# Kernel tuning notes

Hardware: AMD Instinct MI355X
Metric: run time of the kernel (lower is better)

## Reference

```python
import jax, jax.numpy as jnp
import numpy as np

D_MODEL = 64
NUM_MODES = 16
SCALE = 1.0 / (D_MODEL * D_MODEL)


def setup_inputs() -> dict:
    key = jax.random.key(0)
    kq, kk, kv = jax.random.split(key, 3)
    shape = (4, 2048, 64, 64)  # (b, t, c, mw_dim)
    q = jax.random.normal(kq, shape, dtype=jnp.float32)
    k = jax.random.normal(kk, shape, dtype=jnp.float32)
    v = jax.random.normal(kv, shape, dtype=jnp.float32)
    return {"q": q, "k": k, "v": v}


def reference(q, k, v):
    b, t, c, mw = q.shape
    modes = min(t // 2, NUM_MODES)
    # permute (b,t,c,mw) -> (b,h,d,t) with h=mw_dim, d=c
    xq = jnp.transpose(q, (0, 3, 2, 1))
    xk = jnp.transpose(k, (0, 3, 2, 1))
    xv = jnp.transpose(v, (0, 3, 2, 1))
    # rfft over time, keep lowest `modes` frequency bins (contiguous low-pass)
    qf = jnp.fft.rfft(xq, axis=-1)[..., :modes]  # (b,h,d,modes) complex64
    kf = jnp.fft.rfft(xk, axis=-1)[..., :modes]
    vf = jnp.fft.rfft(xv, axis=-1)[..., :modes]
    # complex-domain attention over the reduced mode set
    qk = jnp.einsum('bhdx,bhdy->bhxy', qf, kf)  # (b,h,modes,modes)
    qk = jnp.tanh(qk)  # complex tanh, matching torch.tanh on cfloat
    qkv = jnp.einsum('bhxy,bhdy->bhdx', qk, vf)  # (b,h,d,modes)
    # scatter back into full rfft spectrum (zeros elsewhere)
    out_ft = jnp.zeros((b, mw, c, t // 2 + 1), dtype=qkv.dtype)
    out_ft = out_ft.at[..., :modes].set(qkv)
    out = jnp.fft.irfft(out_ft * SCALE, n=t, axis=-1)  # (b,h,d,t) float32
    return jnp.transpose(out, (0, 3, 2, 1))  # (b,t,c,mw)
```

## Files before the change

kernel.cpp:

```cpp
#include <hip/hip_runtime.h>
#include <hip/hip_bf16.h>
#include <math.h>


#define T_DIM 2048
#define DH 4096
#define DH2 2048
#define CH 8
#define TPCH 64
#define TT 32

__global__ void init_tables(float* __restrict__ WA, float* __restrict__ Bt2) {
    int i = blockIdx.x * 256 + threadIdx.x;
    const float TWO_PI = 6.2831853071795864769f;
    if (i < 512 * 32) {
        int t = i >> 5, r = i & 31, m = r >> 1;
        int ph = (m * t) & 2047;
        float ang = TWO_PI * (float)ph * (1.0f / 2048.0f);
        WA[i] = (r & 1) ? sinf(ang) : cosf(ang);
    }
    int i2 = i - 512 * 32;
    if (i2 >= 0 && i2 < 1024 * 32) {
        int t = i2 >> 5, r = i2 & 31, m = r >> 1;
        int ph = (m * t) & 2047;
        float ang = TWO_PI * (float)ph * (1.0f / 2048.0f);
        const float S2 = 1.0f / (4096.0f * 2048.0f);
        float coef = (m == 0 ? 1.0f : 2.0f) * S2;
        float val;
        if (!(r & 1)) val = coef * cosf(ang);
        else          val = (m == 0) ? 0.0f : -coef * sinf(ang);
        Bt2[i2] = val;
    }
}

__global__ __launch_bounds__(256) void stageA(
        const float* __restrict__ q, const float* __restrict__ k,
        const float* __restrict__ v, const float* __restrict__ WA,
        float* __restrict__ P) {
    __shared__ float w[TPCH * 32];
    int tid = threadIdx.x;
    int c   = blockIdx.y;
    int tz  = blockIdx.z;
    int tensor = tz >> 2, b = tz & 3;

    #pragma unroll
    for (int it = 0; it < TPCH * 32 / 256; it++)
        w[it * 256 + tid] = WA[c * (TPCH * 32) + it * 256 + tid];
    __syncthreads();

    int dh2 = blockIdx.x * 256 + tid;
    const float* srcf = (tensor == 0 ? q : tensor == 1 ? k : v)
                        + (size_t)b * T_DIM * DH;
    const float2* p0 = (const float2*)srcf + (size_t)(c * TPCH) * DH2 + dh2;

    float2 accR[16], accI[16];
    #pragma unroll
    for (int m = 0; m < 16; m++) {
        accR[m] = make_float2(0.f, 0.f);
        accI[m] = make_float2(0.f, 0.f);
    }

    #pragma unroll 2
    for (int tl = 0; tl < TPCH; tl++) {
        float2 x0 = p0[(size_t)tl * DH2];
        float2 x1 = p0[(size_t)(tl + 512) * DH2];
        float2 x2 = p0[(size_t)(tl + 1024) * DH2];
        float2 x3 = p0[(size_t)(tl + 1536) * DH2];
        float2 u0 = make_float2(x0.x + x2.x, x0.y + x2.y);
        float2 u1 = make_float2(x1.x + x3.x, x1.y + x3.y);
        float2 d0 = make_float2(x0.x - x2.x, x0.y - x2.y);
        float2 d1 = make_float2(x1.x - x3.x, x1.y - x3.y);
        float2 e  = make_float2(u0.x + u1.x, u0.y + u1.y);
        float2 f  = make_float2(u0.x - u1.x, u0.y - u1.y);
        const float* ww = &w[tl * 32];
        #pragma unroll
        for (int m = 0; m < 16; m++) {
            float cm = ww[2 * m], sm = ww[2 * m + 1];
            if ((m & 3) == 0) {
                accR[m].x = fmaf(cm, e.x, accR[m].x);
                accR[m].y = fmaf(cm, e.y, accR[m].y);
                accI[m].x = fmaf(-sm, e.x, accI[m].x);
                accI[m].y = fmaf(-sm, e.y, accI[m].y);
            } else if ((m & 3) == 2) {
                accR[m].x = fmaf(cm, f.x, accR[m].x);
                accR[m].y = fmaf(cm, f.y, accR[m].y);
                accI[m].x = fmaf(-sm, f.x, accI[m].x);
                accI[m].y = fmaf(-sm, f.y, accI[m].y);
            } else if ((m & 3) == 1) {
                accR[m].x = fmaf(cm, d0.x, fmaf(-sm, d1.x, accR[m].x));
                accR[m].y = fmaf(cm, d0.y, fmaf(-sm, d1.y, accR[m].y));
                accI[m].x = fmaf(-sm, d0.x, fmaf(-cm, d1.x, accI[m].x));
                accI[m].y = fmaf(-sm, d0.y, fmaf(-cm, d1.y, accI[m].y));
            } else {
                accR[m].x = fmaf(cm, d0.x, fmaf(sm, d1.x, accR[m].x));
                accR[m].y = fmaf(cm, d0.y, fmaf(sm, d1.y, accR[m].y));
                accI[m].x = fmaf(-sm, d0.x, fmaf(cm, d1.x, accI[m].x));
                accI[m].y = fmaf(-sm, d0.y, fmaf(cm, d1.y, accI[m].y));
            }
        }
    }
    float2* pp = (float2*)P + (((size_t)tz * CH + c) * 32) * DH2 + dh2;
    #pragma unroll
    for (int m = 0; m < 16; m++) {
        pp[(size_t)m * DH2]        = accR[m];
        pp[(size_t)(16 + m) * DH2] = accI[m];
    }
}

__global__ __launch_bounds__(256) void reduceP(const float4* __restrict__ P,
                                               float4* __restrict__ Y) {
    size_t i   = (size_t)blockIdx.x * 256 + threadIdx.x;
    size_t tzj = i >> 10;
    size_t dh4 = i & 1023;
    size_t tz  = tzj >> 5;
    size_t j   = tzj & 31;
    const float4* p = P + ((tz * CH) * 32 + j) * 1024 + dh4;
    float4 s = make_float4(0.f, 0.f, 0.f, 0.f);
    #pragma unroll
    for (int cc = 0; cc < CH; cc++) {
        float4 t = p[(size_t)cc * 32 * 1024];
        s.x += t.x; s.y += t.y; s.z += t.z; s.w += t.w;
    }
    Y[i] = s;
}

__global__ __launch_bounds__(256) void stageB(const float* __restrict__ Y,
                                              float* __restrict__ G) {
    __shared__ float qf[64 * 33];
    __shared__ float kf[64 * 33];
    __shared__ float vf[64 * 33];
    __shared__ float qkr[16 * 17];
    __shared__ float qki[16 * 17];

    int tid = threadIdx.x;
    int bh  = blockIdx.x;
    int b   = bh >> 6;
    int h   = bh & 63;

    #pragma unroll
    for (int tensor = 0; tensor < 3; tensor++) {
        float* dst = (tensor == 0 ? qf : tensor == 1 ? kf : vf);
        const float* yp = Y + ((size_t)(tensor * 4 + b) * 32) * DH + h;
        #pragma unroll
        for (int it = 0; it < 8; it++) {
            int p = it * 256 + tid;
            int d = p & 63, j = p >> 6;
            dst[d * 33 + j] = yp[(size_t)j * DH + d * 64];
        }
    }
    __syncthreads();

    int x = tid >> 4, y = tid & 15;
    float ar = 0.f, ai = 0.f;
    #pragma unroll 4
    for (int d = 0; d < 64; d++) {
        float qr = qf[d * 33 + x],      qi = qf[d * 33 + 16 + x];
        float kr = kf[d * 33 + y],      ki = kf[d * 33 + 16 + y];
        ar += qr * kr - qi * ki;
        ai += qr * ki + qi * kr;
    }
    float re, im;
    float a2 = 2.f * ar, b2 = 2.f * ai;
    if (fabsf(a2) < 80.f) {
        float den = coshf(a2) + cosf(b2);
        re = sinhf(a2) / den;
        im = sinf(b2) / den;
    } else {
        re = copysignf(1.f, ar);
        im = 0.f;
    }
    qkr[x * 17 + y] = re;
    qki[x * 17 + y] = im;
    __syncthreads();

    int xx = tid & 15, db = tid >> 4;
    #pragma unroll
    for (int i = 0; i < 4; i++) {
        int d = db + i * 16;
        float cr = 0.f, ci = 0.f;
        #pragma unroll
        for (int yy = 0; yy < 16; yy++) {
            float tr = qkr[xx * 17 + yy], ti = qki[xx * 17 + yy];
            float vr = vf[d * 33 + yy],   vi = vf[d * 33 + 16 + yy];
            cr += tr * vr - ti * vi;
            ci += tr * vi + ti * vr;
        }
        G[((size_t)b * 32 + xx) * DH + d * 64 + h]      = cr;
        G[((size_t)b * 32 + 16 + xx) * DH + d * 64 + h] = ci;
    }
}

__global__ __launch_bounds__(256) void stageC(const float* __restrict__ G,
                                              const float* __restrict__ Bt2,
                                              float* __restrict__ out) {
    __shared__ float w[TT * 32];
    int tid = threadIdx.x;
    int c   = blockIdx.y;
    int b   = blockIdx.z;

    #pragma unroll
    for (int it = 0; it < TT * 32 / 256; it++)
        w[it * 256 + tid] = Bt2[c * (TT * 32) + it * 256 + tid];
    __syncthreads();

    int dh2 = blockIdx.x * 256 + tid;
    float2 gr[16], gi[16];
    const float2* gp = (const float2*)G + (size_t)b * 32 * DH2 + dh2;
    #pragma unroll
    for (int m = 0; m < 16; m++) {
        gr[m] = gp[(size_t)m * DH2];
        gi[m] = gp[(size_t)(16 + m) * DH2];
    }

    float2* o0 = (float2*)out + ((size_t)b * T_DIM + (size_t)c * TT) * DH2 + dh2;
    #pragma unroll 2
    for (int tl = 0; tl < TT; tl++) {
        const float* ww = &w[tl * 32];
        float2 E = make_float2(0.f, 0.f), O = make_float2(0.f, 0.f);
        #pragma unroll
        for (int m = 0; m < 16; m += 2) {
            E.x = fmaf(ww[2 * m],     gr[m].x, E.x);
            E.x = fmaf(ww[2 * m + 1], gi[m].x, E.x);
            E.y = fmaf(ww[2 * m],     gr[m].y, E.y);
            E.y = fmaf(ww[2 * m + 1], gi[m].y, E.y);
        }
        #pragma unroll
        for (int m = 1; m < 16; m += 2) {
            O.x = fmaf(ww[2 * m],     gr[m].x, O.x);
            O.x = fmaf(ww[2 * m + 1], gi[m].x, O.x);
            O.y = fmaf(ww[2 * m],     gr[m].y, O.y);
            O.y = fmaf(ww[2 * m + 1], gi[m].y, O.y);
        }
        o0[(size_t)tl * DH2] = make_float2(E.x + O.x, E.y + O.y);
        o0[(size_t)(tl + 1024) * DH2] = make_float2(E.x - O.x, E.y - O.y);
    }
}

extern "C" void kernel_launch(void* const* d_in, const int* in_sizes, int n_in,
                              void* d_out, int out_size, void* d_ws, size_t ws_size,
                              hipStream_t stream) {
    const float* q = (const float*)d_in[0];
    const float* k = (const float*)d_in[1];
    const float* v = (const float*)d_in[2];
    float* out = (float*)d_out;

    char* ws = (char*)d_ws;
    float* WA  = (float*)ws;
    float* Bt2 = (float*)(ws + 65536);
    float* P   = (float*)(ws + 65536 + 131072);
    float* Y   = (float*)(ws + 65536 + 131072 + 50331648);
    float* G   = (float*)(ws + 65536 + 131072 + 50331648 + 6291456);

    init_tables<<<192, 256, 0, stream>>>(WA, Bt2);
    stageA<<<dim3(8, CH, 12), 256, 0, stream>>>(q, k, v, WA, P);
    reduceP<<<1536, 256, 0, stream>>>((const float4*)P, (float4*)Y);
    stageB<<<256, 256, 0, stream>>>(Y, G);
    stageC<<<dim3(8, 32, 4), 256, 0, stream>>>(G, Bt2, out);
}
```

Before: 448.6 us.

## Increase stageA/stageC grid parallelism and prefetch stageA inputs

StageA is templated on the number of time chunks and launches 16 chunks when the workspace allows it, falling back to 8 otherwise. Its loop now loads the next timestep's inputs before computing the current one, and occupancy hints are added. StageC's time tile is halved so it launches twice as many blocks. The larger split doubles the partial-sum buffer, so reduceP has more memory to read and write.

```diff
diff --git a/kernel.cpp b/kernel.cpp
--- a/kernel.cpp
+++ b/kernel.cpp
@@ -6,9 +6,7 @@
 #define T_DIM 2048
 #define DH 4096
 #define DH2 2048
-#define CH 8
-#define TPCH 64
-#define TT 32
+#define TT 16
 
 __global__ void init_tables(float* __restrict__ WA, float* __restrict__ Bt2) {
     int i = blockIdx.x * 256 + threadIdx.x;
@@ -33,25 +31,62 @@
     }
 }
 
-__global__ __launch_bounds__(256) void stageA(
+#define STAGEA_BODY(TL) do {                                                   \
+    float2 u0 = make_float2(x0.x + x2.x, x0.y + x2.y);                         \
+    float2 u1 = make_float2(x1.x + x3.x, x1.y + x3.y);                         \
+    float2 d0 = make_float2(x0.x - x2.x, x0.y - x2.y);                         \
+    float2 d1 = make_float2(x1.x - x3.x, x1.y - x3.y);                         \
+    float2 e  = make_float2(u0.x + u1.x, u0.y + u1.y);                         \
+    float2 f  = make_float2(u0.x - u1.x, u0.y - u1.y);                         \
+    const float* ww = &w[(TL) * 32];                                           \
+    _Pragma("unroll")                                                          \
+    for (int m = 0; m < 16; m++) {                                             \
+        float cm = ww[2 * m], sm = ww[2 * m + 1];                              \
+        if ((m & 3) == 0) {                                                    \
+            accR[m].x = fmaf(cm, e.x, accR[m].x);                              \
+            accR[m].y = fmaf(cm, e.y, accR[m].y);                              \
+            accI[m].x = fmaf(-sm, e.x, accI[m].x);                             \
+            accI[m].y = fmaf(-sm, e.y, accI[m].y);                             \
+        } else if ((m & 3) == 2) {                                             \
+            accR[m].x = fmaf(cm, f.x, accR[m].x);                              \
+            accR[m].y = fmaf(cm, f.y, accR[m].y);                              \
+            accI[m].x = fmaf(-sm, f.x, accI[m].x);                             \
+            accI[m].y = fmaf(-sm, f.y, accI[m].y);                             \
+        } else if ((m & 3) == 1) {                                             \
+            accR[m].x = fmaf(cm, d0.x, fmaf(-sm, d1.x, accR[m].x));            \
+            accR[m].y = fmaf(cm, d0.y, fmaf(-sm, d1.y, accR[m].y));            \
+            accI[m].x = fmaf(-sm, d0.x, fmaf(-cm, d1.x, accI[m].x));           \
+            accI[m].y = fmaf(-sm, d0.y, fmaf(-cm, d1.y, accI[m].y));           \
+        } else {                                                               \
+            accR[m].x = fmaf(cm, d0.x, fmaf(sm, d1.x, accR[m].x));             \
+            accR[m].y = fmaf(cm, d0.y, fmaf(sm, d1.y, accR[m].y));             \
+            accI[m].x = fmaf(-sm, d0.x, fmaf(cm, d1.x, accI[m].x));            \
+            accI[m].y = fmaf(-sm, d0.y, fmaf(cm, d1.y, accI[m].y));            \
+        }                                                                      \
+    }                                                                          \
+} while (0)
+
+template <int CH_>
+__global__ __launch_bounds__(256, 5) void stageA(
         const float* __restrict__ q, const float* __restrict__ k,
         const float* __restrict__ v, const float* __restrict__ WA,
         float* __restrict__ P) {
-    __shared__ float w[TPCH * 32];
+    constexpr int TPCH_ = 512 / CH_;
+    __shared__ float w[TPCH_ * 32];
     int tid = threadIdx.x;
     int c   = blockIdx.y;
     int tz  = blockIdx.z;
     int tensor = tz >> 2, b = tz & 3;
 
     #pragma unroll
-    for (int it = 0; it < TPCH * 32 / 256; it++)
-        w[it * 256 + tid] = WA[c * (TPCH * 32) + it * 256 + tid];
+    for (int it = 0; it < TPCH_ * 32 / 256; it++)
+        w[it * 256 + tid] = WA[c * (TPCH_ * 32) + it * 256 + tid];
     __syncthreads();
 
     int dh2 = blockIdx.x * 256 + tid;
     const float* srcf = (tensor == 0 ? q : tensor == 1 ? k : v)
                         + (size_t)b * T_DIM * DH;
-    const float2* p0 = (const float2*)srcf + (size_t)(c * TPCH) * DH2 + dh2;
+    const float2* p0 = (const float2*)srcf + (size_t)(c * TPCH_) * DH2 + dh2;
 
     float2 accR[16], accI[16];
     #pragma unroll
@@ -60,46 +95,24 @@
         accI[m] = make_float2(0.f, 0.f);
     }
 
+    float2 x0 = p0[0];
+    float2 x1 = p0[(size_t)512 * DH2];
+    float2 x2 = p0[(size_t)1024 * DH2];
+    float2 x3 = p0[(size_t)1536 * DH2];
+
     #pragma unroll 2
-    for (int tl = 0; tl < TPCH; tl++) {
-        float2 x0 = p0[(size_t)tl * DH2];
-        float2 x1 = p0[(size_t)(tl + 512) * DH2];
-        float2 x2 = p0[(size_t)(tl + 1024) * DH2];
-        float2 x3 = p0[(size_t)(tl + 1536) * DH2];
-        float2 u0 = make_float2(x0.x + x2.x, x0.y + x2.y);
-        float2 u1 = make_float2(x1.x + x3.x, x1.y + x3.y);
-        float2 d0 = make_float2(x0.x - x2.x, x0.y - x2.y);
-        float2 d1 = make_float2(x1.x - x3.x, x1.y - x3.y);
-        float2 e  = make_float2(u0.x + u1.x, u0.y + u1.y);
-        float2 f  = make_float2(u0.x - u1.x, u0.y - u1.y);
-        const float* ww = &w[tl * 32];
-        #pragma unroll
-        for (int m = 0; m < 16; m++) {
-            float cm = ww[2 * m], sm = ww[2 * m + 1];
-            if ((m & 3) == 0) {
-                accR[m].x = fmaf(cm, e.x, accR[m].x);
-                accR[m].y = fmaf(cm, e.y, accR[m].y);
-                accI[m].x = fmaf(-sm, e.x, accI[m].x);
-                accI[m].y = fmaf(-sm, e.y, accI[m].y);
-            } else if ((m & 3) == 2) {
-                accR[m].x = fmaf(cm, f.x, accR[m].x);
-                accR[m].y = fmaf(cm, f.y, accR[m].y);
-                accI[m].x = fmaf(-sm, f.x, accI[m].x);
-                accI[m].y = fmaf(-sm, f.y, accI[m].y);
-            } else if ((m & 3) == 1) {
-                accR[m].x = fmaf(cm, d0.x, fmaf(-sm, d1.x, accR[m].x));
-                accR[m].y = fmaf(cm, d0.y, fmaf(-sm, d1.y, accR[m].y));
-                accI[m].x = fmaf(-sm, d0.x, fmaf(-cm, d1.x, accI[m].x));
-                accI[m].y = fmaf(-sm, d0.y, fmaf(-cm, d1.y, accI[m].y));
-            } else {
-                accR[m].x = fmaf(cm, d0.x, fmaf(sm, d1.x, accR[m].x));
-                accR[m].y = fmaf(cm, d0.y, fmaf(sm, d1.y, accR[m].y));
-                accI[m].x = fmaf(-sm, d0.x, fmaf(cm, d1.x, accI[m].x));
-                accI[m].y = fmaf(-sm, d0.y, fmaf(cm, d1.y, accI[m].y));
-            }
-        }
-    }
-    float2* pp = (float2*)P + (((size_t)tz * CH + c) * 32) * DH2 + dh2;
+    for (int tl = 0; tl < TPCH_ - 1; tl++) {
+        const float2* pn = p0 + (size_t)(tl + 1) * DH2;
+        float2 n0 = pn[0];
+        float2 n1 = pn[(size_t)512 * DH2];
+        float2 n2 = pn[(size_t)1024 * DH2];
+        float2 n3 = pn[(size_t)1536 * DH2];
+        STAGEA_BODY(tl);
+        x0 = n0; x1 = n1; x2 = n2; x3 = n3;
+    }
+    STAGEA_BODY(TPCH_ - 1);
+
+    float2* pp = (float2*)P + (((size_t)tz * CH_ + c) * 32) * DH2 + dh2;
     #pragma unroll
     for (int m = 0; m < 16; m++) {
         pp[(size_t)m * DH2]        = accR[m];
@@ -107,6 +120,7 @@
     }
 }
 
+template <int CH_>
 __global__ __launch_bounds__(256) void reduceP(const float4* __restrict__ P,
                                                float4* __restrict__ Y) {
     size_t i   = (size_t)blockIdx.x * 256 + threadIdx.x;
@@ -114,10 +128,10 @@
     size_t dh4 = i & 1023;
     size_t tz  = tzj >> 5;
     size_t j   = tzj & 31;
-    const float4* p = P + ((tz * CH) * 32 + j) * 1024 + dh4;
+    const float4* p = P + ((tz * CH_) * 32 + j) * 1024 + dh4;
     float4 s = make_float4(0.f, 0.f, 0.f, 0.f);
     #pragma unroll
-    for (int cc = 0; cc < CH; cc++) {
+    for (int cc = 0; cc < CH_; cc++) {
         float4 t = p[(size_t)cc * 32 * 1024];
         s.x += t.x; s.y += t.y; s.z += t.z; s.w += t.w;
     }
@@ -190,9 +204,9 @@
     }
 }
 
-__global__ __launch_bounds__(256) void stageC(const float* __restrict__ G,
-                                              const float* __restrict__ Bt2,
-                                              float* __restrict__ out) {
+__global__ __launch_bounds__(256, 6) void stageC(const float* __restrict__ G,
+                                                 const float* __restrict__ Bt2,
+                                                 float* __restrict__ out) {
     __shared__ float w[TT * 32];
     int tid = threadIdx.x;
     int c   = blockIdx.y;
@@ -247,13 +261,26 @@
     char* ws = (char*)d_ws;
     float* WA  = (float*)ws;
     float* Bt2 = (float*)(ws + 65536);
-    float* P   = (float*)(ws + 65536 + 131072);
-    float* Y   = (float*)(ws + 65536 + 131072 + 50331648);
-    float* G   = (float*)(ws + 65536 + 131072 + 50331648 + 6291456);
+    const size_t base = 65536 + 131072;
+
+    const size_t psz16 = (size_t)12 * 16 * 32 * DH * 4;
+    const size_t psz8  = (size_t)12 *  8 * 32 * DH * 4;
+    const size_t ysz   = 6291456, gsz = 2097152;
+    const bool big = ws_size >= base + psz16 + ysz + gsz;
+
+    size_t psz = big ? psz16 : psz8;
+    float* P = (float*)(ws + base);
+    float* Y = (float*)(ws + base + psz);
+    float* G = (float*)(ws + base + psz + ysz);
 
     init_tables<<<192, 256, 0, stream>>>(WA, Bt2);
-    stageA<<<dim3(8, CH, 12), 256, 0, stream>>>(q, k, v, WA, P);
-    reduceP<<<1536, 256, 0, stream>>>((const float4*)P, (float4*)Y);
+    if (big) {
+        stageA<16><<<dim3(8, 16, 12), 256, 0, stream>>>(q, k, v, WA, P);
+        reduceP<16><<<1536, 256, 0, stream>>>((const float4*)P, (float4*)Y);
+    } else {
+        stageA<8><<<dim3(8, 8, 12), 256, 0, stream>>>(q, k, v, WA, P);
+        reduceP<8><<<1536, 256, 0, stream>>>((const float4*)P, (float4*)Y);
+    }
     stageB<<<256, 256, 0, stream>>>(Y, G);
-    stageC<<<dim3(8, 32, 4), 256, 0, stream>>>(G, Bt2, out);
-}
+    stageC<<<dim3(8, 64, 4), 256, 0, stream>>>(G, Bt2, out);
+}
```

New measurement: 1.290 ms. 188% more time.

## Restructure stageA with float4 loads, LDS double-buffered butterflies, and more blocks

Applied to the files above, without the earlier changes.

StageA now has each wave load float4 rows for a different time step, do the radix-4 butterfly once, and stage the e/f/d0/d1 results in a double-buffered LDS array. Each thread then accumulates one scalar column across the four time steps while the next phase's global loads are in flight. Twiddles are read straight from global memory instead of being staged in shared memory. The grid doubles to 16 blocks per channel with half the accumulators per thread, and stageC's TT is halved with twice the y-blocks. This trades more syncthreads and LDS traffic for wider loads, lower register pressure and more parallelism.

```diff
diff --git a/kernel.cpp b/kernel.cpp
--- a/kernel.cpp
+++ b/kernel.cpp
@@ -8,7 +8,16 @@
 #define DH2 2048
 #define CH 8
 #define TPCH 64
-#define TT 32
+#define NT 4
+#define NPH (TPCH / NT)
+#define TT 16
+
+__device__ inline float4 f4add(float4 a, float4 b) {
+    return make_float4(a.x + b.x, a.y + b.y, a.z + b.z, a.w + b.w);
+}
+__device__ inline float4 f4sub(float4 a, float4 b) {
+    return make_float4(a.x - b.x, a.y - b.y, a.z - b.z, a.w - b.w);
+}
 
 __global__ void init_tables(float* __restrict__ WA, float* __restrict__ Bt2) {
     int i = blockIdx.x * 256 + threadIdx.x;
@@ -37,73 +46,93 @@
         const float* __restrict__ q, const float* __restrict__ k,
         const float* __restrict__ v, const float* __restrict__ WA,
         float* __restrict__ P) {
-    __shared__ float w[TPCH * 32];
-    int tid = threadIdx.x;
-    int c   = blockIdx.y;
-    int tz  = blockIdx.z;
+    __shared__ float elds[2][NT][4][256];
+
+    int tid  = threadIdx.x;
+    int bx   = blockIdx.x;
+    int c    = blockIdx.y;
+    int tz   = blockIdx.z;
     int tensor = tz >> 2, b = tz & 3;
-
-    #pragma unroll
-    for (int it = 0; it < TPCH * 32 / 256; it++)
-        w[it * 256 + tid] = WA[c * (TPCH * 32) + it * 256 + tid];
-    __syncthreads();
-
-    int dh2 = blockIdx.x * 256 + tid;
+    int iw   = tid >> 6;
+    int lane = tid & 63;
+
     const float* srcf = (tensor == 0 ? q : tensor == 1 ? k : v)
                         + (size_t)b * T_DIM * DH;
-    const float2* p0 = (const float2*)srcf + (size_t)(c * TPCH) * DH2 + dh2;
-
-    float2 accR[16], accI[16];
+    const float4* src4 = (const float4*)srcf;
+    int f4base = bx * 64 + lane;
+
+    float accR[16], accI[16];
+    #pragma unroll
+    for (int m = 0; m < 16; m++) { accR[m] = 0.f; accI[m] = 0.f; }
+
+    {
+        int t0 = c * TPCH + iw;
+        float4 x0 = src4[(size_t)t0 * 1024 + f4base];
+        float4 x1 = src4[(size_t)(t0 + 512) * 1024 + f4base];
+        float4 x2 = src4[(size_t)(t0 + 1024) * 1024 + f4base];
+        float4 x3 = src4[(size_t)(t0 + 1536) * 1024 + f4base];
+        float4 u0 = f4add(x0, x2), u1 = f4add(x1, x3);
+        float4 dd0 = f4sub(x0, x2), dd1 = f4sub(x1, x3);
+        ((float4*)&elds[0][iw][0][0])[lane] = f4add(u0, u1);
+        ((float4*)&elds[0][iw][1][0])[lane] = f4sub(u0, u1);
+        ((float4*)&elds[0][iw][2][0])[lane] = dd0;
+        ((float4*)&elds[0][iw][3][0])[lane] = dd1;
+    }
+    __syncthreads();
+
+    for (int ph = 0; ph < NPH; ph++) {
+        float4 n0, n1, n2, n3;
+        const bool has_next = (ph < NPH - 1);
+        if (has_next) {
+            int t0 = c * TPCH + (ph + 1) * NT + iw;
+            n0 = src4[(size_t)t0 * 1024 + f4base];
+            n1 = src4[(size_t)(t0 + 512) * 1024 + f4base];
+            n2 = src4[(size_t)(t0 + 1024) * 1024 + f4base];
+            n3 = src4[(size_t)(t0 + 1536) * 1024 + f4base];
+        }
+        int bsel = ph & 1;
+        #pragma unroll
+        for (int i = 0; i < NT; i++) {
+            float ee  = elds[bsel][i][0][tid];
+            float ff  = elds[bsel][i][1][tid];
+            float dd0 = elds[bsel][i][2][tid];
+            float dd1 = elds[bsel][i][3][tid];
+            const float* tw = WA + (size_t)(c * TPCH + ph * NT + i) * 32;
+            #pragma unroll
+            for (int m = 0; m < 16; m++) {
+                float cm = tw[2 * m], sm = tw[2 * m + 1];
+                if ((m & 3) == 0) {
+                    accR[m] = fmaf(cm, ee, accR[m]);
+                    accI[m] = fmaf(-sm, ee, accI[m]);
+                } else if ((m & 3) == 2) {
+                    accR[m] = fmaf(cm, ff, accR[m]);
+                    accI[m] = fmaf(-sm, ff, accI[m]);
+                } else if ((m & 3) == 1) {
+                    accR[m] = fmaf(cm, dd0, fmaf(-sm, dd1, accR[m]));
+                    accI[m] = fmaf(-sm, dd0, fmaf(-cm, dd1, accI[m]));
+                } else {
+                    accR[m] = fmaf(cm, dd0, fmaf(sm, dd1, accR[m]));
+                    accI[m] = fmaf(-sm, dd0, fmaf(cm, dd1, accI[m]));
+                }
+            }
+        }
+        if (has_next) {
+            int nb = (ph + 1) & 1;
+            float4 u0 = f4add(n0, n2), u1 = f4add(n1, n3);
+            float4 dd0 = f4sub(n0, n2), dd1 = f4sub(n1, n3);
+            ((float4*)&elds[nb][iw][0][0])[lane] = f4add(u0, u1);
+            ((float4*)&elds[nb][iw][1][0])[lane] = f4sub(u0, u1);
+            ((float4*)&elds[nb][iw][2][0])[lane] = dd0;
+            ((float4*)&elds[nb][iw][3][0])[lane] = dd1;
+            __syncthreads();
+        }
+    }
+
+    float* pp = P + ((size_t)(tz * CH + c) * 32) * DH + bx * 256 + tid;
     #pragma unroll
     for (int m = 0; m < 16; m++) {
-        accR[m] = make_float2(0.f, 0.f);
-        accI[m] = make_float2(0.f, 0.f);
-    }
-
-    #pragma unroll 2
-    for (int tl = 0; tl < TPCH; tl++) {
-        float2 x0 = p0[(size_t)tl * DH2];
-        float2 x1 = p0[(size_t)(tl + 512) * DH2];
-        float2 x2 = p0[(size_t)(tl + 1024) * DH2];
-        float2 x3 = p0[(size_t)(tl + 1536) * DH2];
-        float2 u0 = make_float2(x0.x + x2.x, x0.y + x2.y);
-        float2 u1 = make_float2(x1.x + x3.x, x1.y + x3.y);
-        float2 d0 = make_float2(x0.x - x2.x, x0.y - x2.y);
-        float2 d1 = make_float2(x1.x - x3.x, x1.y - x3.y);
-        float2 e  = make_float2(u0.x + u1.x, u0.y + u1.y);
-        float2 f  = make_float2(u0.x - u1.x, u0.y - u1.y);
-        const float* ww = &w[tl * 32];
-        #pragma unroll
-        for (int m = 0; m < 16; m++) {
-            float cm = ww[2 * m], sm = ww[2 * m + 1];
-            if ((m & 3) == 0) {
-                accR[m].x = fmaf(cm, e.x, accR[m].x);
-                accR[m].y = fmaf(cm, e.y, accR[m].y);
-                accI[m].x = fmaf(-sm, e.x, accI[m].x);
-                accI[m].y = fmaf(-sm, e.y, accI[m].y);
-            } else if ((m & 3) == 2) {
-                accR[m].x = fmaf(cm, f.x, accR[m].x);
-                accR[m].y = fmaf(cm, f.y, accR[m].y);
-                accI[m].x = fmaf(-sm, f.x, accI[m].x);
-                accI[m].y = fmaf(-sm, f.y, accI[m].y);
-            } else if ((m & 3) == 1) {
-                accR[m].x = fmaf(cm, d0.x, fmaf(-sm, d1.x, accR[m].x));
-                accR[m].y = fmaf(cm, d0.y, fmaf(-sm, d1.y, accR[m].y));
-                accI[m].x = fmaf(-sm, d0.x, fmaf(-cm, d1.x, accI[m].x));
-                accI[m].y = fmaf(-sm, d0.y, fmaf(-cm, d1.y, accI[m].y));
-            } else {
-                accR[m].x = fmaf(cm, d0.x, fmaf(sm, d1.x, accR[m].x));
-                accR[m].y = fmaf(cm, d0.y, fmaf(sm, d1.y, accR[m].y));
-                accI[m].x = fmaf(-sm, d0.x, fmaf(cm, d1.x, accI[m].x));
-                accI[m].y = fmaf(-sm, d0.y, fmaf(cm, d1.y, accI[m].y));
-            }
-        }
-    }
-    float2* pp = (float2*)P + (((size_t)tz * CH + c) * 32) * DH2 + dh2;
-    #pragma unroll
-    for (int m = 0; m < 16; m++) {
-        pp[(size_t)m * DH2]        = accR[m];
-        pp[(size_t)(16 + m) * DH2] = accI[m];
+        pp[(size_t)m * DH]        = accR[m];
+        pp[(size_t)(16 + m) * DH] = accI[m];
     }
 }
 
@@ -247,13 +276,17 @@
     char* ws = (char*)d_ws;
     float* WA  = (float*)ws;
     float* Bt2 = (float*)(ws + 65536);
-    float* P   = (float*)(ws + 65536 + 131072);
-    float* Y   = (float*)(ws + 65536 + 131072 + 50331648);
-    float* G   = (float*)(ws + 65536 + 131072 + 50331648 + 6291456);
+    const size_t base = 65536 + 131072;
+
+    const size_t psz = (size_t)12 * CH * 32 * DH * 4;
+    const size_t ysz = 6291456;
+    float* P = (float*)(ws + base);
+    float* Y = (float*)(ws + base + psz);
+    float* G = (float*)(ws + base + psz + ysz);
 
     init_tables<<<192, 256, 0, stream>>>(WA, Bt2);
-    stageA<<<dim3(8, CH, 12), 256, 0, stream>>>(q, k, v, WA, P);
+    stageA<<<dim3(16, CH, 12), 256, 0, stream>>>(q, k, v, WA, P);
     reduceP<<<1536, 256, 0, stream>>>((const float4*)P, (float4*)Y);
     stageB<<<256, 256, 0, stream>>>(Y, G);
-    stageC<<<dim3(8, 32, 4), 256, 0, stream>>>(G, Bt2, out);
-}
+    stageC<<<dim3(8, 64, 4), 256, 0, stream>>>(G, Bt2, out);
+}
```

After: 435.4 us. 1.03x faster.
